# Kernel tuning notes

Hardware: AMD Instinct MI355X
Metric: run time of the kernel (lower is better)

## Reference

```python
import jax, jax.numpy as jnp
import numpy as np

N_HEADS = 12
LN_EPS = 1e-5


def _layernorm(x, w):
    # torch F.layer_norm (no affine) then * w
    x = x.astype(jnp.float32)
    mu = jnp.mean(x, axis=-1, keepdims=True)
    var = jnp.mean(jnp.square(x - mu), axis=-1, keepdims=True)
    return (x - mu) * jax.lax.rsqrt(var + LN_EPS) * w


def _rotate_half(x):
    x1, x2 = jnp.split(x, 2, axis=-1)
    return jnp.concatenate([-x2, x1], axis=-1)


def setup_inputs() -> dict:
    key = jax.random.key(0)
    ks = jax.random.split(key, 10)
    b, s, dim, cond, hd = 2, 4096, 768, 768, 64
    mlp = 4 * dim
    # rotary tables
    inv_freq = 1.0 / (10000.0 ** (np.arange(0, hd, 2, dtype=np.float32) / hd))
    t = np.arange(s, dtype=np.float32)
    freqs = np.einsum('s,d->sd', t, inv_freq)           # [s, hd/2]
    emb = np.concatenate([freqs, freqs], axis=-1)        # [s, hd]
    cos = jnp.asarray(np.cos(emb))[None, :, None, None, :]
    sin = jnp.asarray(np.sin(emb))[None, :, None, None, :]
    sc = lambda f: 1.0 / np.sqrt(f)
    return {
        'x': jax.random.normal(ks[0], (b, s, dim), jnp.float32),
        'cos': cos,
        'sin': sin,
        'c': jax.random.normal(ks[1], (b, cond), jnp.float32),
        'attention_mask': jax.random.randint(ks[2], (b, s), 0, 2, jnp.int32),
        'ln1_w': jnp.ones((dim,), jnp.float32),
        'Wqkv': jax.random.normal(ks[3], (3 * dim, dim), jnp.float32) * sc(dim),
        'Wout': jax.random.normal(ks[4], (dim, dim), jnp.float32) * sc(dim),
        'ln2_w': jnp.ones((dim,), jnp.float32),
        'W1': jax.random.normal(ks[5], (mlp, dim), jnp.float32) * sc(dim),
        'b1': jnp.zeros((mlp,), jnp.float32),
        'W2': jax.random.normal(ks[6], (dim, mlp), jnp.float32) * sc(mlp),
        'b2': jnp.zeros((dim,), jnp.float32),
        'Wada': jax.random.normal(ks[7], (6 * dim, cond), jnp.float32) * 0.02,
        'bada': jnp.zeros((6 * dim,), jnp.float32),
    }


def reference(x, cos, sin, c, attention_mask, ln1_w, Wqkv, Wout, ln2_w, W1, b1, W2, b2, Wada, bada):
    b, s, dim = x.shape
    h, hd = N_HEADS, dim // N_HEADS
    # adaLN modulation: [b, 6*dim] -> six [b, 1, dim] chunks
    mod = (c @ Wada.T + bada)[:, None, :]
    shift_msa, scale_msa, gate_msa, shift_mlp, scale_mlp, gate_mlp = jnp.split(mod, 6, axis=2)

    x_skip = x
    hdn = _layernorm(x, ln1_w) * (1.0 + scale_msa) + shift_msa
    qkv = (hdn @ Wqkv.T).reshape(b, s, 3, h, hd)
    qkv = qkv * cos + _rotate_half(qkv) * sin            # RoPE on q, k, and v (as in source)
    q = jnp.transpose(qkv[:, :, 0], (0, 2, 1, 3))        # [b, h, s, hd]
    k = jnp.transpose(qkv[:, :, 1], (0, 2, 1, 3))
    v = jnp.transpose(qkv[:, :, 2], (0, 2, 1, 3))

    m = attention_mask.astype(bool)
    pair = m[:, None, :, None] & m[:, None, None, :]     # [b, 1, s, s]
    bias = jnp.where(pair, 0.0, -1e9).astype(q.dtype)

    scores = jnp.einsum('bhqd,bhkd->bhqk', q, k) / jnp.sqrt(jnp.asarray(hd, q.dtype))
    attn = jax.nn.softmax(scores + bias, axis=-1)
    o = jnp.einsum('bhqk,bhkd->bhqd', attn, v)
    o = jnp.transpose(o, (0, 2, 1, 3)).reshape(b, s, dim)

    # inference-mode bias_dropout_add_scale (dropout off)
    x = x_skip + gate_msa * (o @ Wout.T)
    h2 = _layernorm(x, ln2_w) * (1.0 + scale_mlp) + shift_mlp
    mlp = jax.nn.gelu(h2 @ W1.T + b1, approximate=True) @ W2.T + b2
    return x + gate_mlp * mlp
```

## Files before the change

### kernel.cpp

```cpp
#include <hip/hip_runtime.h>
#include <stdint.h>


typedef unsigned short u16;
typedef __attribute__((ext_vector_type(4))) float f32x4;
typedef __attribute__((ext_vector_type(8))) short short8;
typedef __attribute__((ext_vector_type(4))) short s16x4;
typedef __attribute__((ext_vector_type(8))) __bf16 bf16x8;

__device__ __forceinline__ float b2f(u16 u){
  union { unsigned int i; float f; } v; v.i = ((unsigned int)u) << 16; return v.f;
}
__device__ __forceinline__ u16 f2b(float f){
  union { float f; unsigned int i; } v; v.f = f;
  unsigned int u = v.i;
  u = u + 0x7FFFu + ((u >> 16) & 1u);
  return (u16)(u >> 16);
}
__device__ __forceinline__ f32x4 mfma16(short8 a, short8 b, f32x4 c){
  return __builtin_amdgcn_mfma_f32_16x16x32_bf16(
      __builtin_bit_cast(bf16x8, a), __builtin_bit_cast(bf16x8, b), c, 0, 0, 0);
}
__device__ __forceinline__ void gload16(const void* g, void* l){
  void* gnc = const_cast<void*>(g);
  __builtin_amdgcn_global_load_lds((__attribute__((address_space(1))) void*)gnc,
                                   (__attribute__((address_space(3))) void*)l, 16, 0, 0);
}

__global__ __launch_bounds__(256) void cvt4_k(
    const float* __restrict__ s0, u16* __restrict__ d0,
    const float* __restrict__ s1, u16* __restrict__ d1,
    const float* __restrict__ s2, u16* __restrict__ d2,
    const float* __restrict__ s3, u16* __restrict__ d3)
{
  int i = blockIdx.x*256 + threadIdx.x;
  const float* src; u16* dst; int j = i;
  if (j < 442368){ src = s0; dst = d0; }
  else if ((j -= 442368) < 147456){ src = s1; dst = d1; }
  else if ((j -= 147456) < 589824){ src = s2; dst = d2; }
  else { j -= 589824; src = s3; dst = d3; }
  float4 v = *(const float4*)(src + (size_t)j*4);
  s16x4 o; o[0]=(short)f2b(v.x); o[1]=(short)f2b(v.y);
  o[2]=(short)f2b(v.z); o[3]=(short)f2b(v.w);
  *(s16x4*)(dst + (size_t)j*4) = o;
}

__global__ __launch_bounds__(256) void kbias_k(const int* __restrict__ mask,
                                               float* __restrict__ kb,
                                               float* __restrict__ vm, int n)
{
  int i = blockIdx.x*256 + threadIdx.x;
  if (i < n) kb[i] = mask[i] ? -32.f : -1e30f;
  if (i < 24*64) vm[i] = 0.f;
}

__global__ __launch_bounds__(256) void mod_k(const float* __restrict__ c,
    const float* __restrict__ Wada, const float* __restrict__ bada, float* __restrict__ modb)
{
  int o = blockIdx.x*4 + (threadIdx.x >> 6);
  int l = threadIdx.x & 63;
  int b = o / 4608, j = o - b*4608;
  const float* cp = c + b*768;
  const float* wp = Wada + (size_t)j*768;
  float s = 0.f;
  for (int k = l; k < 768; k += 64) s += cp[k] * wp[k];
  #pragma unroll
  for (int d=1; d<64; d<<=1) s += __shfl_xor(s, d);
  if (l == 0) modb[o] = s + bada[j];
}

__global__ __launch_bounds__(256) void ln_mod_k(const float* __restrict__ xin,
    u16* __restrict__ out, const float* __restrict__ lnw, const float* __restrict__ modb,
    int shift_c, int scale_c)
{
  int row = blockIdx.x;
  int b = row >> 12;
  const float* xp = xin + (size_t)row*768;
  int t = threadIdx.x;
  float v[3]; float s = 0.f, s2 = 0.f;
  #pragma unroll
  for (int i=0;i<3;i++){ float f = xp[t + i*256]; v[i] = f; s += f; s2 += f*f; }
  #pragma unroll
  for (int d=1; d<64; d<<=1){ s += __shfl_xor(s, d); s2 += __shfl_xor(s2, d); }
  __shared__ float rs_[4], rs2_[4];
  int w = t >> 6;
  if ((t & 63) == 0){ rs_[w] = s; rs2_[w] = s2; }
  __syncthreads();
  s  = rs_[0]+rs_[1]+rs_[2]+rs_[3];
  s2 = rs2_[0]+rs2_[1]+rs2_[2]+rs2_[3];
  float mu  = s * (1.f/768.f);
  float var = fmaxf(s2 * (1.f/768.f) - mu*mu, 0.f);
  float rstd = rsqrtf(var + 1e-5f);
  const float* scp = modb + b*4608 + scale_c*768;
  const float* shp = modb + b*4608 + shift_c*768;
  #pragma unroll
  for (int i=0;i<3;i++){
    int d = t + i*256;
    float f = (v[i]-mu)*rstd*lnw[d];
    f = f*(1.f + scp[d]) + shp[d];
    out[(size_t)row*768 + d] = f2b(f);
  }
}

template<int EPI>
__global__ __launch_bounds__(256) void gemm_k(
    const u16* __restrict__ A, const u16* __restrict__ Bt, void* __restrict__ Cv,
    int M, int N, int K,
    const float* __restrict__ addend, const float* __restrict__ modb,
    const float* __restrict__ bias,
    const float* __restrict__ cosb, const float* __restrict__ sinb,
    u16* __restrict__ qO, u16* __restrict__ kO, u16* __restrict__ vO)
{
  __shared__ __align__(16) u16 As[128*64];
  __shared__ __align__(16) u16 Bs[128*64];
  const int bm = blockIdx.x, bn = blockIdx.y;
  const int tid = threadIdx.x;
  const int w = tid >> 6, l = tid & 63;
  const int wr = w >> 1, wc = w & 1;
  const int l15 = l & 15, lg = l >> 4;
  f32x4 acc[4][4] = {};

  for (int k0 = 0; k0 < K; k0 += 64){
    #pragma unroll
    for (int i=0;i<4;i++){
      int e = i*256 + tid;
      int r = e >> 3, ch = e & 7;
      int sc = ch ^ (r & 7);
      gload16(A  + (size_t)(bm*128 + r)*K + k0 + sc*8, &As[e*8]);
      gload16(Bt + (size_t)(bn*128 + r)*K + k0 + sc*8, &Bs[e*8]);
    }
    __syncthreads();
    #pragma unroll
    for (int kk=0;kk<2;kk++){
      short8 af[4], bfv[4];
      #pragma unroll
      for (int i=0;i<4;i++){
        int ra = wr*64 + i*16 + l15;
        af[i]  = *(const short8*)&As[ra*64 + (((kk*4)+lg) ^ (ra&7))*8];
        int rb = wc*64 + i*16 + l15;
        bfv[i] = *(const short8*)&Bs[rb*64 + (((kk*4)+lg) ^ (rb&7))*8];
      }
      #pragma unroll
      for (int m=0;m<4;m++)
        #pragma unroll
        for (int n=0;n<4;n++)
          acc[m][n] = mfma16(af[m], bfv[n], acc[m][n]);
    }
    __syncthreads();
  }

  if constexpr (EPI == 4){
    const int colseg = bn*128 + wc*64;
    const int qi = colseg / 768;
    const int h  = (colseg - qi*768) >> 6;
    const float qs = (qi == 0) ? 0.1803368801111601f : 1.f;
    u16* dst = (qi == 0) ? qO : (qi == 1) ? kO : vO;
    #pragma unroll
    for (int m=0;m<4;m++){
      #pragma unroll
      for (int r=0;r<4;r++){
        int row = bm*128 + wr*64 + m*16 + lg*4 + r;
        int s = row & 4095, bb = row >> 12;
        size_t obase = ((size_t)(bb*12 + h)*4096 + s)*64;
        #pragma unroll
        for (int n2=0;n2<2;n2++){
          int d1 = n2*16 + l15;
          int d2 = d1 + 32;
          float c1 = cosb[s*64 + d1], s1 = sinb[s*64 + d1];
          float c2 = cosb[s*64 + d2], s2 = sinb[s*64 + d2];
          float x1 = acc[m][n2][r], x2 = acc[m][n2+2][r];
          dst[obase + d1] = f2b((x1*c1 - x2*s1)*qs);
          dst[obase + d2] = f2b((x2*c2 + x1*s2)*qs);
        }
      }
    }
    return;
  }

  #pragma unroll
  for (int m=0;m<4;m++){
    int row0 = bm*128 + wr*64 + m*16 + lg*4;
    #pragma unroll
    for (int n=0;n<4;n++){
      int col = bn*128 + wc*64 + n*16 + l15;
      #pragma unroll
      for (int r=0;r<4;r++){
        int row = row0 + r;
        size_t idx = (size_t)row*N + col;
        float v = acc[m][n][r];
        if constexpr (EPI == 0){
          ((u16*)Cv)[idx] = f2b(v);
        } else if constexpr (EPI == 1){
          float g = modb[(row>>12)*4608 + 2*768 + col];
          ((float*)Cv)[idx] = addend[idx] + g*v;
        } else if constexpr (EPI == 2){
          float u = v + bias[col];
          float t0 = 0.7978845608028654f*(u + 0.044715f*u*u*u);
          ((u16*)Cv)[idx] = f2b(0.5f*u*(1.0f + tanhf(t0)));
        } else if constexpr (EPI == 3){
          float g = modb[(row>>12)*4608 + 5*768 + col];
          float u = v + bias[col];
          ((float*)Cv)[idx] = addend[idx] + g*u;
        }
      }
    }
  }
}

__global__ __launch_bounds__(256) void vtr_k(const u16* __restrict__ vS,
                                             u16* __restrict__ vT,
                                             float* __restrict__ vm)
{
  __shared__ __align__(16) u16 tile[64][72];
  __shared__ float cs[4][64];
  int st = blockIdx.x, bh = blockIdx.y;
  int t = threadIdx.x;
  #pragma unroll
  for (int i=0;i<2;i++){
    int e = i*256 + t;
    int r = e >> 3, d0 = (e & 7)*8;
    short8 vv = *(const short8*)(vS + ((size_t)bh*4096 + st*64 + r)*64 + d0);
    *(short8*)&tile[r][d0] = vv;
  }
  __syncthreads();
  #pragma unroll
  for (int i=0;i<2;i++){
    int e = i*256 + t;
    int d = e >> 3, s0 = (e & 7)*8;
    short8 ov;
    #pragma unroll
    for (int k2=0;k2<8;k2++) ov[k2] = (short)tile[s0+k2][d];
    *(short8*)(vT + ((size_t)bh*64 + d)*4096 + st*64 + s0) = ov;
  }
  int d = t & 63, qq = t >> 6;
  float s = 0.f;
  #pragma unroll
  for (int i=0;i<16;i++) s += b2f(tile[qq*16 + i][d]);
  cs[qq][d] = s;
  __syncthreads();
  if (qq == 0) atomicAdd(&vm[bh*64 + d], cs[0][d]+cs[1][d]+cs[2][d]+cs[3][d]);
}

#define AT_BODY(KT, KQK, KST, VPV, VST, STC, STN)                              \
{                                                                              \
  f32x4 kb_[4];                                                                \
  _Pragma("unroll")                                                            \
  for (int n=0;n<4;n++)                                                        \
    kb_[n] = *(const f32x4*)(kbrow + (KT)*64 + n*16 + lg*4);                   \
  __builtin_amdgcn_sched_barrier(0);       \
  { int k3 = (KT)+3 < kend ? (KT)+3 : kend-1;                                  \
    gload16(kbase + (size_t)(k3*64+sr)*64 + ssc*8, &Ks[KST][tid*8]); }         \
  { int v2 = (KT)+2 < kend ? (KT)+2 : kend-1;                                  \
    gload16(vbase + (size_t)sr*4096 + v2*64 + ssc*8, &Vs[VST][tid*8]); }       \
  if ((KT)+1 < kend){                                                          \
    __builtin_amdgcn_s_setprio(1);                                             \
    _Pragma("unroll")                                                          \
    for (int n=0;n<4;n++){                                                     \
      int R = n*16 + l15;                                                      \
      f32x4 a_ = {};                                                           \
      _Pragma("unroll")                                                        \
      for (int kk=0;kk<2;kk++){                                                \
        short8 ka = *(const short8*)&Ks[KQK][R*64 + (((kk<<2)+lg) ^ (R&7))*8]; \
        a_ = mfma16(ka, bq[kk], a_);                                           \
      }                                                                        \
      STN[n] = a_;                                                             \
    }                                                                          \
    __builtin_amdgcn_s_setprio(0);                                             \
  }                                                                            \
              \
  float p_[4][4]; float ts_ = 0.f;                                             \
  _Pragma("unroll")                                                            \
  for (int n=0;n<4;n++)                                                        \
    _Pragma("unroll")                                                          \
    for (int r=0;r<4;r++){                                                     \
      float e_ = __builtin_amdgcn_exp2f(STC[n][r] + kb_[n][r]);                \
      p_[n][r] = e_; ts_ += e_;                                                \
    }                                                                          \
  ts_ += __shfl_xor(ts_, 16);                                                  \
  ts_ += __shfl_xor(ts_, 32);                                                  \
  l_run += ts_;                                                                \
  _Pragma("unroll")                                                            \
  for (int n=0;n<4;n++){                                                       \
    unsigned p01_, p23_;                                                       \
    asm("v_cvt_pk_bf16_f32 %0, %1, %2" : "=v"(p01_) : "v"(p_[n][0]), "v"(p_[n][1])); \
    asm("v_cvt_pk_bf16_f32 %0, %1, %2" : "=v"(p23_) : "v"(p_[n][2]), "v"(p_[n][3])); \
    int s0_ = n*16 + lg*4;                                                     \
    int off_ = (((s0_>>3) ^ (l15&7))<<3) + (s0_&7);                            \
    *(unsigned*)&Ps[w][l15*64 + off_]     = p01_;                              \
    *(unsigned*)&Ps[w][l15*64 + off_ + 2] = p23_;                              \
  }                                                                            \
  __builtin_amdgcn_s_setprio(1);                                               \
  _Pragma("unroll")                                                            \
  for (int kk=0;kk<2;kk++){                                                    \
    int ch_ = (kk<<2) + lg;                                                    \
    short8 bp_ = *(const short8*)&Ps[w][l15*64 + ((ch_ ^ (l15&7))<<3)];        \
    _Pragma("unroll")                                                          \
    for (int n=0;n<4;n++){                                                     \
      int R = n*16 + l15;                                                      \
      short8 va_ = *(const short8*)&Vs[VPV][R*64 + ((ch_ ^ (R&7))<<3)];        \
      oacc[n] = mfma16(va_, bp_, oacc[n]);                                     \
    }                                                                          \
  }                                                                            \
  __builtin_amdgcn_s_setprio(0);                                               \
  __builtin_amdgcn_s_barrier();                                                \
}

__global__ __launch_bounds__(512) void attn_k(
    const u16* __restrict__ qT, const u16* __restrict__ kT, const u16* __restrict__ vT,
    const float* __restrict__ kbias, float* __restrict__ po, float* __restrict__ pl)
{
  __shared__ __align__(16) u16 Ks[4][64*64];
  __shared__ __align__(16) u16 Vs[4][64*64];
  __shared__ __align__(16) u16 Ps[8][16*64];
  const int qt = blockIdx.x, bh = blockIdx.y, kv = blockIdx.z;
  const int b = bh / 12;
  const int tid = threadIdx.x, w = tid >> 6, l = tid & 63;
  const int l15 = l & 15, lg = l >> 4;
  const int k0 = kv*32, kend = k0 + 32;

  short8 bq[2];
  {
    const u16* qp = qT + ((size_t)bh*4096 + qt*128 + w*16 + l15)*64 + lg*8;
    bq[0] = *(const short8*)qp;
    bq[1] = *(const short8*)(qp + 32);
  }
  const float* kbrow = kbias + b*4096 + k0*64;
  const u16* kbase = kT + (size_t)bh*4096*64 + (size_t)k0*64*64;
  const u16* vbase = vT + (size_t)bh*64*4096 + (size_t)k0*64;

  float l_run = 0.f;
  f32x4 oacc[4] = {};

  const int sr = tid >> 3, ssc = (tid & 7) ^ (sr & 7);

  gload16(kbase + (size_t)sr*64 + ssc*8,            &Ks[0][tid*8]);
  gload16(kbase + (size_t)(64+sr)*64 + ssc*8,       &Ks[1][tid*8]);
  gload16(kbase + (size_t)(128+sr)*64 + ssc*8,      &Ks[2][tid*8]);
  gload16(vbase + (size_t)sr*4096 + ssc*8,          &Vs[0][tid*8]);
  gload16(vbase + (size_t)sr*4096 + 64 + ssc*8,     &Vs[1][tid*8]);
  asm volatile("s_waitcnt vmcnt(0)" ::: "memory");
  __builtin_amdgcn_s_barrier();

  f32x4 stA[4], stB[4];
  #pragma unroll
  for (int n=0;n<4;n++){
    int R = n*16 + l15;
    f32x4 a_ = {};
    #pragma unroll
    for (int kk=0;kk<2;kk++){
      short8 ka = *(const short8*)&Ks[0][R*64 + (((kk<<2)+lg) ^ (R&7))*8];
      a_ = mfma16(ka, bq[kk], a_);
    }
    stA[n] = a_;
  }

  for (int kt = 0; kt < 32; kt += 4){
    AT_BODY(kt+0, 1, 3, 0, 2, stA, stB)
    AT_BODY(kt+1, 2, 0, 1, 3, stB, stA)
    AT_BODY(kt+2, 3, 1, 2, 0, stA, stB)
    AT_BODY(kt+3, 0, 2, 3, 1, stB, stA)
  }

  const int qrow = qt*128 + w*16 + l15;
  float* pob = po + (((size_t)kv*24 + bh)*4096 + qrow)*64;
  #pragma unroll
  for (int n=0;n<4;n++)
    *(f32x4*)&pob[n*16 + lg*4] = oacc[n];
  if (lg == 0) pl[((size_t)kv*24 + bh)*4096 + qrow] = l_run;
}

__global__ __launch_bounds__(256) void comb_k(const float* __restrict__ po,
    const float* __restrict__ pl, const int* __restrict__ mask,
    const float* __restrict__ vm, u16* __restrict__ o)
{
  int row = blockIdx.x;
  int b = row >> 12, s = row & 4095;
  bool fq = mask[row] != 0;
  int t = threadIdx.x;
  #pragma unroll
  for (int i=0;i<3;i++){
    int j = t + i*256;
    int h = j >> 6, d = j & 63;
    size_t pi = (((size_t)b*12 + h)*4096 + s)*64 + d;
    size_t li = ((size_t)b*12 + h)*4096 + s;
    float O = po[pi] + po[(size_t)24*4096*64 + pi];
    float L = pl[li] + pl[(size_t)24*4096 + li];
    float v = fq ? O / L : vm[(b*12 + h)*64 + d]*(1.f/4096.f);
    o[(size_t)row*768 + j] = f2b(v);
  }
}

extern "C" void kernel_launch(void* const* d_in, const int* in_sizes, int n_in,
                              void* d_out, int out_size, void* d_ws, size_t ws_size,
                              hipStream_t stream)
{
  const float* x    = (const float*)d_in[0];
  const float* cosb = (const float*)d_in[1];
  const float* sinb = (const float*)d_in[2];
  const float* c    = (const float*)d_in[3];
  const int* amask  = (const int*)d_in[4];
  const float* ln1w = (const float*)d_in[5];
  const float* Wqkv = (const float*)d_in[6];
  const float* Wout = (const float*)d_in[7];
  const float* ln2w = (const float*)d_in[8];
  const float* W1   = (const float*)d_in[9];
  const float* b1   = (const float*)d_in[10];
  const float* W2   = (const float*)d_in[11];
  const float* b2   = (const float*)d_in[12];
  const float* Wada = (const float*)d_in[13];
  const float* bada = (const float*)d_in[14];

  char* ws = (char*)d_ws;
  size_t off = 0;
  auto take = [&](size_t bytes)->char*{
    char* p = ws + off; off = (off + bytes + 255) & ~(size_t)255; return p;
  };
  float* modb = (float*)take(9216*sizeof(float));
  float* kbias= (float*)take(8192*sizeof(float));
  float* vmean= (float*)take(24*64*sizeof(float));
  u16* hdn  = (u16*)take((size_t)8192*768*2);
  u16* bufA = (u16*)take((size_t)8192*3072*2);
  u16* vS   = (u16*)take((size_t)8192*768*2);
  u16* qTb  = (u16*)take((size_t)8192*768*2);
  u16* kTb  = (u16*)take((size_t)8192*768*2);
  u16* vTb  = (u16*)take((size_t)8192*768*2);
  u16* ob   = (u16*)take((size_t)8192*768*2);
  u16* WqkvB= (u16*)take((size_t)2304*768*2);
  u16* WoutB= (u16*)take((size_t)768*768*2);
  u16* W1B  = (u16*)take((size_t)3072*768*2);
  u16* W2B  = (u16*)take((size_t)768*3072*2);
  float* out = (float*)d_out;
  float* x1 = out;
  float* po = (float*)bufA;
  float* pl = (float*)hdn;

  cvt4_k<<<6912, 256, 0, stream>>>(Wqkv, WqkvB, Wout, WoutB, W1, W1B, W2, W2B);
  kbias_k<<<32, 256, 0, stream>>>(amask, kbias, vmean, 8192);

  mod_k  <<<2304, 256, 0, stream>>>(c, Wada, bada, modb);
  ln_mod_k<<<8192, 256, 0, stream>>>(x, hdn, ln1w, modb, 0, 1);
  gemm_k<4><<<dim3(64,18), 256, 0, stream>>>(hdn, WqkvB, nullptr, 8192, 2304, 768,
                                             nullptr, nullptr, nullptr,
                                             cosb, sinb, qTb, kTb, vS);
  vtr_k  <<<dim3(64,24), 256, 0, stream>>>(vS, vTb, vmean);
  attn_k <<<dim3(32,24,2), 512, 0, stream>>>(qTb, kTb, vTb, kbias, po, pl);
  comb_k <<<8192, 256, 0, stream>>>(po, pl, amask, vmean, ob);
  gemm_k<1><<<dim3(64,6), 256, 0, stream>>>(ob, WoutB, x1, 8192, 768, 768,
                                            x, modb, nullptr,
                                            nullptr, nullptr, nullptr, nullptr, nullptr);
  ln_mod_k<<<8192, 256, 0, stream>>>(x1, hdn, ln2w, modb, 3, 4);
  gemm_k<2><<<dim3(64,24), 256, 0, stream>>>(hdn, W1B, bufA, 8192, 3072, 768,
                                             nullptr, nullptr, b1,
                                             nullptr, nullptr, nullptr, nullptr, nullptr);
  gemm_k<3><<<dim3(64,6), 256, 0, stream>>>(bufA, W2B, out, 8192, 768, 3072,
                                            x1, modb, b2,
                                            nullptr, nullptr, nullptr, nullptr, nullptr);
}
```

Baseline: 396.6 us.

## Compact valid keys via mask scan and run attention only over them

A per-batch ballot scan builds an index list of unmasked key positions and a count. A gather kernel packs K and transposed V for only those positions, zero-padded to a multiple of 512, and a separate kernel computes the V column sums. The attention kernel then loops over just the padded count of compacted key tiles instead of all 4096 keys, aiming to skip the masked half of the QK and PV work. The cost is an extra gather pass, a serial single-wave scan kernel, and a changed key bias constant (0 instead of -32) that shifts the exp2 range.

```diff
diff --git a/kernel.cpp b/kernel.cpp
--- a/kernel.cpp
+++ b/kernel.cpp
@@ -45,13 +45,23 @@
   *(s16x4*)(dst + (size_t)j*4) = o;
 }
 
-__global__ __launch_bounds__(256) void kbias_k(const int* __restrict__ mask,
-                                               float* __restrict__ kb,
-                                               float* __restrict__ vm, int n)
-{
-  int i = blockIdx.x*256 + threadIdx.x;
-  if (i < n) kb[i] = mask[i] ? -32.f : -1e30f;
-  if (i < 24*64) vm[i] = 0.f;
+__global__ __launch_bounds__(64) void scan_k(const int* __restrict__ mask,
+    int* __restrict__ idx, int* __restrict__ nvalid, float* __restrict__ kbc,
+    float* __restrict__ vm)
+{
+  int b = blockIdx.x, l = threadIdx.x;
+  const int* m = mask + b*4096;
+  int base = 0;
+  for (int i0 = 0; i0 < 4096; i0 += 64){
+    int v = m[i0 + l] != 0;
+    unsigned long long bal = __ballot(v);
+    int pre = __popcll(bal & ((1ull << l) - 1ull));
+    if (v) idx[b*4096 + base + pre] = i0 + l;
+    base += (int)__popcll(bal);
+  }
+  if (l == 0) nvalid[b] = base;
+  for (int i = l; i < 4096; i += 64) kbc[b*4096 + i] = (i < base) ? 0.f : -1e30f;
+  if (b == 0) for (int i = l; i < 24*64; i += 64) vm[i] = 0.f;
 }
 
 __global__ __launch_bounds__(256) void mod_k(const float* __restrict__ c,
@@ -207,38 +217,54 @@
   }
 }
 
-__global__ __launch_bounds__(256) void vtr_k(const u16* __restrict__ vS,
-                                             u16* __restrict__ vT,
-                                             float* __restrict__ vm)
+__global__ __launch_bounds__(256) void gath_k(const u16* __restrict__ kT,
+    const u16* __restrict__ vS, const int* __restrict__ idx,
+    const int* __restrict__ nvalid, u16* __restrict__ kc, u16* __restrict__ vTc)
 {
   __shared__ __align__(16) u16 tile[64][72];
-  __shared__ float cs[4][64];
-  int st = blockIdx.x, bh = blockIdx.y;
+  int j0 = blockIdx.x*64, bh = blockIdx.y;
+  int b = bh / 12;
+  int nv = nvalid[b];
+  int npad = (nv + 511) & ~511;
+  if (j0 >= npad) return;
   int t = threadIdx.x;
   #pragma unroll
   for (int i=0;i<2;i++){
     int e = i*256 + t;
-    int r = e >> 3, d0 = (e & 7)*8;
-    short8 vv = *(const short8*)(vS + ((size_t)bh*4096 + st*64 + r)*64 + d0);
-    *(short8*)&tile[r][d0] = vv;
+    int r = e >> 3, ch = e & 7;
+    int j = j0 + r;
+    short8 kv8 = {}, vv8 = {};
+    if (j < nv){
+      int src = idx[b*4096 + j];
+      kv8 = *(const short8*)(kT + ((size_t)bh*4096 + src)*64 + ch*8);
+      vv8 = *(const short8*)(vS + ((size_t)bh*4096 + src)*64 + ch*8);
+    }
+    *(short8*)(kc + ((size_t)bh*4096 + j)*64 + ch*8) = kv8;
+    *(short8*)&tile[r][ch*8] = vv8;
   }
   __syncthreads();
   #pragma unroll
   for (int i=0;i<2;i++){
     int e = i*256 + t;
-    int d = e >> 3, s0 = (e & 7)*8;
+    int dd = e >> 3, s0 = (e & 7)*8;
     short8 ov;
     #pragma unroll
-    for (int k2=0;k2<8;k2++) ov[k2] = (short)tile[s0+k2][d];
-    *(short8*)(vT + ((size_t)bh*64 + d)*4096 + st*64 + s0) = ov;
-  }
-  int d = t & 63, qq = t >> 6;
+    for (int k2=0;k2<8;k2++) ov[k2] = (short)tile[s0+k2][dd];
+    *(short8*)(vTc + ((size_t)bh*64 + dd)*4096 + j0 + s0) = ov;
+  }
+}
+
+__global__ __launch_bounds__(256) void vmean2_k(const u16* __restrict__ vS,
+                                                float* __restrict__ vm)
+{
+  int bh = blockIdx.y, r0 = blockIdx.x*256;
+  int t = threadIdx.x, d = t & 63, g = t >> 6;
+  const u16* p = vS + ((size_t)bh*4096 + r0)*64 + d;
   float s = 0.f;
-  #pragma unroll
-  for (int i=0;i<16;i++) s += b2f(tile[qq*16 + i][d]);
-  cs[qq][d] = s;
-  __syncthreads();
-  if (qq == 0) atomicAdd(&vm[bh*64 + d], cs[0][d]+cs[1][d]+cs[2][d]+cs[3][d]);
+  for (int k = g; k < 256; k += 4) s += b2f(p[(size_t)k*64]);
+  __shared__ float red[4][64];
+  red[g][d] = s; __syncthreads();
+  if (g == 0) atomicAdd(&vm[bh*64 + d], red[0][d]+red[1][d]+red[2][d]+red[3][d]);
 }
 
 #define AT_BODY(KT, KQK, KST, VPV, VST, STC, STN)                              \
@@ -248,11 +274,11 @@
   for (int n=0;n<4;n++)                                                        \
     kb_[n] = *(const f32x4*)(kbrow + (KT)*64 + n*16 + lg*4);                   \
   __builtin_amdgcn_sched_barrier(0);       \
-  { int k3 = (KT)+3 < kend ? (KT)+3 : kend-1;                                  \
+  { int k3 = (KT)+3 < bodies ? (KT)+3 : bodies-1;                              \
     gload16(kbase + (size_t)(k3*64+sr)*64 + ssc*8, &Ks[KST][tid*8]); }         \
-  { int v2 = (KT)+2 < kend ? (KT)+2 : kend-1;                                  \
+  { int v2 = (KT)+2 < bodies ? (KT)+2 : bodies-1;                              \
     gload16(vbase + (size_t)sr*4096 + v2*64 + ssc*8, &Vs[VST][tid*8]); }       \
-  if ((KT)+1 < kend){                                                          \
+  if ((KT)+1 < bodies){                                                        \
     __builtin_amdgcn_s_setprio(1);                                             \
     _Pragma("unroll")                                                          \
     for (int n=0;n<4;n++){                                                     \
@@ -267,7 +293,6 @@
     }                                                                          \
     __builtin_amdgcn_s_setprio(0);                                             \
   }                                                                            \
-              \
   float p_[4][4]; float ts_ = 0.f;                                             \
   _Pragma("unroll")                                                            \
   for (int n=0;n<4;n++)                                                        \
@@ -306,8 +331,9 @@
 }
 
 __global__ __launch_bounds__(512) void attn_k(
-    const u16* __restrict__ qT, const u16* __restrict__ kT, const u16* __restrict__ vT,
-    const float* __restrict__ kbias, float* __restrict__ po, float* __restrict__ pl)
+    const u16* __restrict__ qT, const u16* __restrict__ kc, const u16* __restrict__ vTc,
+    const float* __restrict__ kbc, const int* __restrict__ nvalid,
+    float* __restrict__ po, float* __restrict__ pl)
 {
   __shared__ __align__(16) u16 Ks[4][64*64];
   __shared__ __align__(16) u16 Vs[4][64*64];
@@ -316,7 +342,9 @@
   const int b = bh / 12;
   const int tid = threadIdx.x, w = tid >> 6, l = tid & 63;
   const int l15 = l & 15, lg = l >> 4;
-  const int k0 = kv*32, kend = k0 + 32;
+  const int nv = nvalid[b];
+  const int bodies = ((nv + 511) & ~511) >> 7;
+  const int k0 = kv * bodies;
 
   short8 bq[2];
   {
@@ -324,9 +352,9 @@
     bq[0] = *(const short8*)qp;
     bq[1] = *(const short8*)(qp + 32);
   }
-  const float* kbrow = kbias + b*4096 + k0*64;
-  const u16* kbase = kT + (size_t)bh*4096*64 + (size_t)k0*64*64;
-  const u16* vbase = vT + (size_t)bh*64*4096 + (size_t)k0*64;
+  const float* kbrow = kbc + b*4096 + k0*64;
+  const u16* kbase = kc + ((size_t)bh*4096 + (size_t)k0*64)*64;
+  const u16* vbase = vTc + (size_t)bh*64*4096 + (size_t)k0*64;
 
   float l_run = 0.f;
   f32x4 oacc[4] = {};
@@ -354,7 +382,7 @@
     stA[n] = a_;
   }
 
-  for (int kt = 0; kt < 32; kt += 4){
+  for (int kt = 0; kt < bodies; kt += 4){
     AT_BODY(kt+0, 1, 3, 0, 2, stA, stB)
     AT_BODY(kt+1, 2, 0, 1, 3, stB, stA)
     AT_BODY(kt+2, 3, 1, 2, 0, stA, stB)
@@ -416,14 +444,17 @@
     char* p = ws + off; off = (off + bytes + 255) & ~(size_t)255; return p;
   };
   float* modb = (float*)take(9216*sizeof(float));
-  float* kbias= (float*)take(8192*sizeof(float));
+  float* kbc  = (float*)take(8192*sizeof(float));
   float* vmean= (float*)take(24*64*sizeof(float));
+  int*   idx  = (int*)take(8192*sizeof(int));
+  int*   nvld = (int*)take(2*sizeof(int));
   u16* hdn  = (u16*)take((size_t)8192*768*2);
   u16* bufA = (u16*)take((size_t)8192*3072*2);
   u16* vS   = (u16*)take((size_t)8192*768*2);
   u16* qTb  = (u16*)take((size_t)8192*768*2);
   u16* kTb  = (u16*)take((size_t)8192*768*2);
-  u16* vTb  = (u16*)take((size_t)8192*768*2);
+  u16* kc   = (u16*)take((size_t)8192*768*2);
+  u16* vTc  = (u16*)take((size_t)8192*768*2);
   u16* ob   = (u16*)take((size_t)8192*768*2);
   u16* WqkvB= (u16*)take((size_t)2304*768*2);
   u16* WoutB= (u16*)take((size_t)768*768*2);
@@ -435,15 +466,16 @@
   float* pl = (float*)hdn;
 
   cvt4_k<<<6912, 256, 0, stream>>>(Wqkv, WqkvB, Wout, WoutB, W1, W1B, W2, W2B);
-  kbias_k<<<32, 256, 0, stream>>>(amask, kbias, vmean, 8192);
+  scan_k<<<2, 64, 0, stream>>>(amask, idx, nvld, kbc, vmean);
 
   mod_k  <<<2304, 256, 0, stream>>>(c, Wada, bada, modb);
   ln_mod_k<<<8192, 256, 0, stream>>>(x, hdn, ln1w, modb, 0, 1);
   gemm_k<4><<<dim3(64,18), 256, 0, stream>>>(hdn, WqkvB, nullptr, 8192, 2304, 768,
                                              nullptr, nullptr, nullptr,
                                              cosb, sinb, qTb, kTb, vS);
-  vtr_k  <<<dim3(64,24), 256, 0, stream>>>(vS, vTb, vmean);
-  attn_k <<<dim3(32,24,2), 512, 0, stream>>>(qTb, kTb, vTb, kbias, po, pl);
+  gath_k <<<dim3(64,24), 256, 0, stream>>>(kTb, vS, idx, nvld, kc, vTc);
+  vmean2_k<<<dim3(16,24), 256, 0, stream>>>(vS, vmean);
+  attn_k <<<dim3(32,24,2), 512, 0, stream>>>(qTb, kc, vTc, kbc, nvld, po, pl);
   comb_k <<<8192, 256, 0, stream>>>(po, pl, amask, vmean, ob);
   gemm_k<1><<<dim3(64,6), 256, 0, stream>>>(ob, WoutB, x1, 8192, 768, 768,
                                             x, modb, nullptr,
```

Measured after the change: 368.6 us. 1.08x faster.
